# Performance work log

Hardware: AMD Instinct MI355X
Metric: run time of the kernel (lower is better)

## Reference

```python
import jax, jax.numpy as jnp
import numpy as np


def _coord1d(n):
    # make_coord: grid-center coordinates in (-1, 1)
    return -1.0 + 1.0 / n + (2.0 / n) * jnp.arange(n, dtype=jnp.float32)


def _conv1x1(x, w, b):
    # 1x1 conv == channel matmul. x: [B,C,H,W], w: [O,C], b: [O]
    return jnp.einsum('bchw,oc->bohw', x, w) + b[None, :, None, None]


def setup_inputs() -> dict:
    key = jax.random.key(0)
    ks = jax.random.split(key, 8)
    B, C, h, w = 2, 64, 96, 96
    d = 256
    Cin = (C + 2) * 4 + 2  # 266
    s = lambda k, shp, fan: (jax.random.normal(k, shp, jnp.float32) / np.sqrt(fan)).astype(jnp.float32)
    return {
        'feat': jax.random.normal(ks[0], (B, C, h, w), jnp.float32),
        'w00': s(ks[1], (d, Cin), Cin), 'b00': jnp.zeros((d,), jnp.float32),
        'w1': s(ks[2], (d, d), d), 'b1': jnp.zeros((d,), jnp.float32),
        'w2': s(ks[3], (3, d), d), 'b2': jnp.zeros((3,), jnp.float32),
        'ws1': s(ks[4], (C, C), C), 'bs1': jnp.zeros((C,), jnp.float32),
        'ws2': s(ks[5], (3, C), C), 'bs2': jnp.zeros((3,), jnp.float32),
        'target_h': 384, 'target_w': 384,
    }


def reference(feat, w00, b00, w1, b1, w2, b2, ws1, bs1, ws2, bs2, target_h, target_w):
    B, C, h, w = feat.shape
    H, W = int(target_h), int(target_w)
    # HR query coordinates, shared across batch. cy along height (dim0), cx along width (dim1)
    cy = jnp.broadcast_to(_coord1d(H)[:, None], (H, W))
    cx = jnp.broadcast_to(_coord1d(W)[None, :], (H, W))
    rx = 1.0 / h  # = 2/h/2, half-pixel radius along height
    ry = 1.0 / w
    eps_shift = 1e-6

    def nearest(c, n):
        # grid_sample nearest, align_corners=False: unnormalize then round (half-to-even, as nearbyint)
        u = ((c + 1.0) * n - 1.0) / 2.0
        return jnp.clip(jnp.round(u).astype(jnp.int32), 0, n - 1)

    rel_coords, feat_s, areas = [], [], []
    for vx in (-1.0, 1.0):
        for vy in (-1.0, 1.0):
            sy = jnp.clip(cy + vx * rx + eps_shift, -1.0 + 1e-6, 1.0 - 1e-6)
            sx = jnp.clip(cx + vy * ry + eps_shift, -1.0 + 1e-6, 1.0 - 1e-6)
            iy = nearest(sy, h)  # [H,W]
            ix = nearest(sx, w)
            feat_s.append(feat[:, :, iy, ix])  # [B,C,H,W] gather
            # nearest-sampled LR pixel-center coords (what grid_sample(pos_lr,...) returns)
            old_y = -1.0 + 1.0 / h + (2.0 / h) * iy.astype(jnp.float32)
            old_x = -1.0 + 1.0 / w + (2.0 / w) * ix.astype(jnp.float32)
            rel_y = (cy - old_y) * h
            rel_x = (cx - old_x) * w
            rel_coords.append(jnp.stack([rel_y, rel_x], 0))  # [2,H,W]
            areas.append(jnp.abs(rel_y * rel_x) + 1e-9)

    tot = areas[0] + areas[1] + areas[2] + areas[3]
    # LIIF area swap: 0<->3, 1<->2
    areas = [areas[3], areas[2], areas[1], areas[0]]
    feat_s = [f * (a / tot)[None, None] for f, a in zip(feat_s, areas)]

    scale_h, scale_w = H / h, W / w
    cell_h = (2.0 / H) * max(scale_h / 4.0, 1.0) * h
    cell_w = (2.0 / W) * max(scale_w / 4.0, 1.0) * w
    rel_cell = jnp.broadcast_to(
        jnp.array([cell_h, cell_w], jnp.float32)[None, :, None, None], (B, 2, H, W))
    rels = jnp.broadcast_to(jnp.concatenate(rel_coords, 0)[None], (B, 8, H, W))
    grid = jnp.concatenate([rels, *feat_s, rel_cell], axis=1)  # [B,266,H,W]

    x = _conv1x1(grid, w00, b00)
    ret = _conv1x1(jax.nn.gelu(_conv1x1(x, w1, b1), approximate=False), w2, b2)

    # shortcut branch: 1x1 MLP on LR feat, then bilinear border sample at coord
    sc = _conv1x1(jax.nn.relu(_conv1x1(feat, ws1, bs1)), ws2, bs2)  # [B,3,h,w]
    uy = ((cy + 1.0) * h - 1.0) / 2.0
    ux = ((cx + 1.0) * w - 1.0) / 2.0
    y0 = jnp.floor(uy)
    x0 = jnp.floor(ux)
    wy = uy - y0
    wx = ux - x0
    y0i = jnp.clip(y0.astype(jnp.int32), 0, h - 1)
    y1i = jnp.clip(y0.astype(jnp.int32) + 1, 0, h - 1)
    x0i = jnp.clip(x0.astype(jnp.int32), 0, w - 1)
    x1i = jnp.clip(x0.astype(jnp.int32) + 1, 0, w - 1)
    samp = (sc[:, :, y0i, x0i] * ((1 - wy) * (1 - wx))[None, None]
            + sc[:, :, y0i, x1i] * ((1 - wy) * wx)[None, None]
            + sc[:, :, y1i, x0i] * (wy * (1 - wx))[None, None]
            + sc[:, :, y1i, x1i] * (wy * wx)[None, None])
    return ret + samp
```

## Files before the change

kernel.cpp:

```cpp
#include <hip/hip_runtime.h>

typedef __bf16 bf16x8 __attribute__((ext_vector_type(8)));
typedef __bf16 bf16x4 __attribute__((ext_vector_type(4)));
typedef float f32x4 __attribute__((ext_vector_type(4)));

namespace {
constexpr int Bn = 2, Cn = 64, hn = 96, wn = 96, Hn = 384, Wn = 384;
constexpr int CIN = 266;
constexpr int TM = 64;
constexpr int SP = 296;
constexpr int L1_FRAGS = 9 * 16 * 64;
constexpr int L2_FRAGS = 8 * 16 * 64;
constexpr int L3_FRAGS = 8 * 64;
constexpr int N_FRAGS = L1_FRAGS + L2_FRAGS + L3_FRAGS;
constexpr int SC_OFF_BYTES = N_FRAGS * 16;
constexpr int B1EFF_OFF_BYTES = SC_OFF_BYTES + Bn * 3 * hn * wn * 4;
constexpr int FRAG_BLOCKS = N_FRAGS / 256;
constexpr int SC_BLOCKS = (Bn * hn * wn) / 256;
}

__global__ void prep_all(const float* __restrict__ w00, const float* __restrict__ w1,
                         const float* __restrict__ w2, const float* __restrict__ b00,
                         const float* __restrict__ b1,
                         const float* __restrict__ feat, const float* __restrict__ ws1,
                         const float* __restrict__ bs1, const float* __restrict__ ws2,
                         const float* __restrict__ bs2,
                         __bf16* __restrict__ wb, float* __restrict__ b1eff,
                         float* __restrict__ sc)
{
    const int bid = blockIdx.x;
    if (bid < FRAG_BLOCKS) {
        const int f = bid * 256 + threadIdx.x;
        bf16x8 v;
        if (f < L1_FRAGS) {
            const int k0 = f >> 10;
            const int mb = (f >> 6) & 15;
            const int l  = f & 63;
            const int m  = mb * 16 + (l & 15);
            const int kb = k0 * 32 + (l >> 4) * 8;
#pragma unroll
            for (int j = 0; j < 8; j++)
                v[j] = (kb + j < CIN) ? (__bf16)w00[m * CIN + kb + j] : (__bf16)0.f;
        } else if (f < L1_FRAGS + L2_FRAGS) {
            const int g = f - L1_FRAGS;
            const int k0 = g >> 10;
            const int mb = (g >> 6) & 15;
            const int l  = g & 63;
            const int m  = mb * 16 + (l & 15);
            const int kb = k0 * 32 + (l >> 4) * 8;
#pragma unroll
            for (int j = 0; j < 8; j++) v[j] = (__bf16)w1[m * 256 + kb + j];
        } else {
            const int g = f - (L1_FRAGS + L2_FRAGS);
            const int k0 = g >> 6;
            const int l  = g & 63;
            const int m  = l & 15;
            const int kb = k0 * 32 + (l >> 4) * 8;
#pragma unroll
            for (int j = 0; j < 8; j++)
                v[j] = (m < 3) ? (__bf16)w2[m * 256 + kb + j] : (__bf16)0.f;
        }
        *(bf16x8*)(wb + f * 8) = v;
        return;
    }
    if (bid == FRAG_BLOCKS) {
        __shared__ float cb[256];
        const int o = threadIdx.x;
        cb[o] = b00[o] + 0.5f * (w00[o * CIN + 264] + w00[o * CIN + 265]);
        __syncthreads();
        float v = b1[o];
#pragma unroll 4
        for (int k = 0; k < 256; k++) v = fmaf(w1[o * 256 + k], cb[k], v);
        b1eff[o] = v;
        return;
    }
    const int t = (bid - FRAG_BLOCKS - 1) * 256 + threadIdx.x;
    if (t >= Bn * hn * wn) return;
    const int b = t / (hn * wn);
    const int yx = t % (hn * wn);
    const float* fp = feat + b * Cn * hn * wn + yx;
    float f[Cn];
#pragma unroll
    for (int c = 0; c < Cn; c++) f[c] = fp[c * hn * wn];
    float o0 = bs2[0], o1 = bs2[1], o2 = bs2[2];
#pragma unroll 1
    for (int co = 0; co < Cn; co += 4) {
        float v0 = bs1[co], v1 = bs1[co + 1], v2 = bs1[co + 2], v3 = bs1[co + 3];
        const float* wr = ws1 + co * Cn;
#pragma unroll
        for (int ci = 0; ci < Cn; ci++) {
            const float fv = f[ci];
            v0 = fmaf(wr[ci], fv, v0);
            v1 = fmaf(wr[Cn + ci], fv, v1);
            v2 = fmaf(wr[2 * Cn + ci], fv, v2);
            v3 = fmaf(wr[3 * Cn + ci], fv, v3);
        }
        v0 = fmaxf(v0, 0.f); v1 = fmaxf(v1, 0.f); v2 = fmaxf(v2, 0.f); v3 = fmaxf(v3, 0.f);
#pragma unroll
        for (int u = 0; u < 4; u++) {
            const float vv = (u == 0) ? v0 : (u == 1) ? v1 : (u == 2) ? v2 : v3;
            o0 = fmaf(ws2[co + u], vv, o0);
            o1 = fmaf(ws2[Cn + co + u], vv, o1);
            o2 = fmaf(ws2[2 * Cn + co + u], vv, o2);
        }
    }
    sc[(b * 3 + 0) * hn * wn + yx] = o0;
    sc[(b * 3 + 1) * hn * wn + yx] = o1;
    sc[(b * 3 + 2) * hn * wn + yx] = o2;
}

__device__ __forceinline__ float gelu_fast(float x) {
    const float d0 = -2.302118074f;
    const float d1 = -0.1029453754f;
    float t = x * x;
    float a = x * fmaf(t, d1, d0);
    float e = __builtin_amdgcn_exp2f(a);
    return x * __builtin_amdgcn_rcpf(1.f + e);
}

__device__ __forceinline__ bf16x4 pack4(f32x4 x) {
    bf16x4 v;
    v[0] = (__bf16)x[0]; v[1] = (__bf16)x[1]; v[2] = (__bf16)x[2]; v[3] = (__bf16)x[3];
    return v;
}


#define MF(A, B, C) __builtin_amdgcn_mfma_f32_16x16x32_bf16((A), (B), (C), 0, 0, 0)

#define GSTEP(k0, W0, W1, W2, W3) do {                                          \
    const bf16x8 g0 = *(const bf16x8*)&Abuf[     lane16][(k0) * 32 + quad * 8]; \
    const bf16x8 g1 = *(const bf16x8*)&Abuf[16 + lane16][(k0) * 32 + quad * 8]; \
    const bf16x8 g2 = *(const bf16x8*)&Abuf[32 + lane16][(k0) * 32 + quad * 8]; \
    const bf16x8 g3 = *(const bf16x8*)&Abuf[48 + lane16][(k0) * 32 + quad * 8]; \
    a00 = MF(W0, g0, a00); a01 = MF(W1, g0, a01); a02 = MF(W2, g0, a02); a03 = MF(W3, g0, a03); \
    a10 = MF(W0, g1, a10); a11 = MF(W1, g1, a11); a12 = MF(W2, g1, a12); a13 = MF(W3, g1, a13); \
    a20 = MF(W0, g2, a20); a21 = MF(W1, g2, a21); a22 = MF(W2, g2, a22); a23 = MF(W3, g2, a23); \
    a30 = MF(W0, g3, a30); a31 = MF(W1, g3, a31); a32 = MF(W2, g3, a32); a33 = MF(W3, g3, a33); \
} while (0)

#define LDW(W0, W1, W2, W3, src, kk) do {             \
    W0 = (src)[((kk) * 16 + mb0 + 0) * 64 + lane];    \
    W1 = (src)[((kk) * 16 + mb0 + 1) * 64 + lane];    \
    W2 = (src)[((kk) * 16 + mb0 + 2) * 64 + lane];    \
    W3 = (src)[((kk) * 16 + mb0 + 3) * 64 + lane];    \
} while (0)

#define ZACC4(n) a##n##0 = zf; a##n##1 = zf; a##n##2 = zf; a##n##3 = zf

__global__ __launch_bounds__(256, 3) void liif_main(
    const float* __restrict__ feat, const float* __restrict__ b1eff,
    const float* __restrict__ b2v, const __bf16* __restrict__ wb,
    const float* __restrict__ sc, float* __restrict__ out)
{
    __shared__ __align__(16) __bf16 Abuf[TM][SP];

    const int t = threadIdx.x;
    const int wv = t >> 6;
    const int lane = t & 63;
    const int lane16 = lane & 15;
    const int quad = lane >> 4;
    const int mb0 = wv * 4;

    constexpr int NWG = Bn * Hn * (Wn / TM);
    const int lt = (blockIdx.x & 7) * (NWG / 8) + (blockIdx.x >> 3);
    constexpr int TPR = Wn / TM;
    const int tx = lt % TPR;
    const int Y = (lt / TPR) % Hn;
    const int b = lt / (TPR * Hn);
    const int X0 = tx * TM;

    const float cy = -1.f + 1.f / Hn + (2.f / Hn) * (float)Y;

    const bf16x8* wf1 = (const bf16x8*)wb;
    const bf16x8* wf2 = wf1 + L1_FRAGS;
    const bf16x8* w2f = wf1 + (L1_FRAGS + L2_FRAGS);

    bf16x8 wE0, wE1, wE2, wE3, wO0, wO1, wO2, wO3;
    LDW(wE0, wE1, wE2, wE3, wf1, 0);
    LDW(wO0, wO1, wO2, wO3, wf1, 1);

    {
        const int p = lane;
        const int j = wv;
        const int X = X0 + p;
        const float cx = -1.f + 1.f / Wn + (2.f / Wn) * (float)X;
        float rely[4], relx[4], area[4];
        int iyv[4], ixv[4];
#pragma unroll
        for (int c = 0; c < 4; c++) {
            const float vx = (c & 2) ? 1.f : -1.f;
            const float vy = (c & 1) ? 1.f : -1.f;
            float sy = fminf(fmaxf(cy + vx * (1.f / hn) + 1e-6f, -1.f + 1e-6f), 1.f - 1e-6f);
            float sx = fminf(fmaxf(cx + vy * (1.f / wn) + 1e-6f, -1.f + 1e-6f), 1.f - 1e-6f);
            float uy = ((sy + 1.f) * hn - 1.f) * 0.5f;
            float ux = ((sx + 1.f) * wn - 1.f) * 0.5f;
            int iy = min(max((int)rintf(uy), 0), hn - 1);
            int ix = min(max((int)rintf(ux), 0), wn - 1);
            float oy = -1.f + 1.f / hn + (2.f / hn) * (float)iy;
            float ox = -1.f + 1.f / wn + (2.f / wn) * (float)ix;
            rely[c] = (cy - oy) * hn;
            relx[c] = (cx - ox) * wn;
            area[c] = fabsf(rely[c] * relx[c]) + 1e-9f;
            iyv[c] = iy; ixv[c] = ix;
        }
        const float tot = area[0] + area[1] + area[2] + area[3];
        const float wj = area[3 - j] / tot;

        if (j == 0) {
            bf16x8 v;
#pragma unroll
            for (int c = 0; c < 4; c++) { v[2 * c] = (__bf16)rely[c]; v[2 * c + 1] = (__bf16)relx[c]; }
            *(bf16x8*)&Abuf[p][0] = v;
        }
        const float* fb = feat + ((b * Cn) * hn + iyv[j]) * wn + ixv[j];
#pragma unroll
        for (int c8 = 0; c8 < 8; c8++) {
            bf16x8 v;
#pragma unroll
            for (int cc = 0; cc < 8; cc++)
                v[cc] = (__bf16)(fb[(c8 * 8 + cc) * (hn * wn)] * wj);
            *(bf16x8*)&Abuf[p][8 + 64 * j + c8 * 8] = v;
        }
        if (j == 3) {
            bf16x8 z;
#pragma unroll
            for (int cc = 0; cc < 8; cc++) z[cc] = (__bf16)0.f;
            *(bf16x8*)&Abuf[p][264] = z;
            *(bf16x8*)&Abuf[p][272] = z;
            *(bf16x8*)&Abuf[p][280] = z;
        }
    }
    __syncthreads();

    const f32x4 zf = (f32x4){0.f, 0.f, 0.f, 0.f};
    f32x4 a00, a01, a02, a03, a10, a11, a12, a13;
    f32x4 a20, a21, a22, a23, a30, a31, a32, a33;
    ZACC4(0); ZACC4(1); ZACC4(2); ZACC4(3);

    GSTEP(0, wE0, wE1, wE2, wE3); LDW(wE0, wE1, wE2, wE3, wf1, 2);
    GSTEP(1, wO0, wO1, wO2, wO3); LDW(wO0, wO1, wO2, wO3, wf1, 3);
    GSTEP(2, wE0, wE1, wE2, wE3); LDW(wE0, wE1, wE2, wE3, wf1, 4);
    GSTEP(3, wO0, wO1, wO2, wO3); LDW(wO0, wO1, wO2, wO3, wf1, 5);
    GSTEP(4, wE0, wE1, wE2, wE3); LDW(wE0, wE1, wE2, wE3, wf1, 6);
    GSTEP(5, wO0, wO1, wO2, wO3); LDW(wO0, wO1, wO2, wO3, wf1, 7);
    GSTEP(6, wE0, wE1, wE2, wE3); LDW(wE0, wE1, wE2, wE3, wf1, 8);
    GSTEP(7, wO0, wO1, wO2, wO3); LDW(wO0, wO1, wO2, wO3, wf2, 0);
    GSTEP(8, wE0, wE1, wE2, wE3); LDW(wE0, wE1, wE2, wE3, wf2, 1);

    __syncthreads();
    {
        const int ch0 = mb0 * 16 + quad * 4;
        *(bf16x4*)&Abuf[     lane16][ch0     ] = pack4(a00);
        *(bf16x4*)&Abuf[16 + lane16][ch0     ] = pack4(a10);
        *(bf16x4*)&Abuf[32 + lane16][ch0     ] = pack4(a20);
        *(bf16x4*)&Abuf[48 + lane16][ch0     ] = pack4(a30);
        *(bf16x4*)&Abuf[     lane16][ch0 + 16] = pack4(a01);
        *(bf16x4*)&Abuf[16 + lane16][ch0 + 16] = pack4(a11);
        *(bf16x4*)&Abuf[32 + lane16][ch0 + 16] = pack4(a21);
        *(bf16x4*)&Abuf[48 + lane16][ch0 + 16] = pack4(a31);
        *(bf16x4*)&Abuf[     lane16][ch0 + 32] = pack4(a02);
        *(bf16x4*)&Abuf[16 + lane16][ch0 + 32] = pack4(a12);
        *(bf16x4*)&Abuf[32 + lane16][ch0 + 32] = pack4(a22);
        *(bf16x4*)&Abuf[48 + lane16][ch0 + 32] = pack4(a32);
        *(bf16x4*)&Abuf[     lane16][ch0 + 48] = pack4(a03);
        *(bf16x4*)&Abuf[16 + lane16][ch0 + 48] = pack4(a13);
        *(bf16x4*)&Abuf[32 + lane16][ch0 + 48] = pack4(a23);
        *(bf16x4*)&Abuf[48 + lane16][ch0 + 48] = pack4(a33);
    }
    __syncthreads();

    ZACC4(0); ZACC4(1); ZACC4(2); ZACC4(3);

    GSTEP(0, wO0, wO1, wO2, wO3); LDW(wO0, wO1, wO2, wO3, wf2, 2);
    GSTEP(1, wE0, wE1, wE2, wE3); LDW(wE0, wE1, wE2, wE3, wf2, 3);
    GSTEP(2, wO0, wO1, wO2, wO3); LDW(wO0, wO1, wO2, wO3, wf2, 4);
    GSTEP(3, wE0, wE1, wE2, wE3); LDW(wE0, wE1, wE2, wE3, wf2, 5);
    GSTEP(4, wO0, wO1, wO2, wO3); LDW(wO0, wO1, wO2, wO3, wf2, 6);
    GSTEP(5, wE0, wE1, wE2, wE3); LDW(wE0, wE1, wE2, wE3, wf2, 7);
    GSTEP(6, wO0, wO1, wO2, wO3); wO0 = w2f[0 * 64 + lane];
    GSTEP(7, wE0, wE1, wE2, wE3); wE0 = w2f[1 * 64 + lane];

    __syncthreads();
    {
        const int ch0 = mb0 * 16 + quad * 4;
        const f32x4 bi0 = *(const f32x4*)&b1eff[ch0];
        const f32x4 bi1 = *(const f32x4*)&b1eff[ch0 + 16];
        const f32x4 bi2 = *(const f32x4*)&b1eff[ch0 + 32];
        const f32x4 bi3 = *(const f32x4*)&b1eff[ch0 + 48];
#define GEL4(x, bi) { bf16x4 v; v[0] = (__bf16)gelu_fast((x)[0] + (bi)[0]); \
        v[1] = (__bf16)gelu_fast((x)[1] + (bi)[1]); \
        v[2] = (__bf16)gelu_fast((x)[2] + (bi)[2]); \
        v[3] = (__bf16)gelu_fast((x)[3] + (bi)[3]); vv = v; }
        bf16x4 vv;
        GEL4(a00, bi0); *(bf16x4*)&Abuf[     lane16][ch0     ] = vv;
        GEL4(a10, bi0); *(bf16x4*)&Abuf[16 + lane16][ch0     ] = vv;
        GEL4(a20, bi0); *(bf16x4*)&Abuf[32 + lane16][ch0     ] = vv;
        GEL4(a30, bi0); *(bf16x4*)&Abuf[48 + lane16][ch0     ] = vv;
        GEL4(a01, bi1); *(bf16x4*)&Abuf[     lane16][ch0 + 16] = vv;
        GEL4(a11, bi1); *(bf16x4*)&Abuf[16 + lane16][ch0 + 16] = vv;
        GEL4(a21, bi1); *(bf16x4*)&Abuf[32 + lane16][ch0 + 16] = vv;
        GEL4(a31, bi1); *(bf16x4*)&Abuf[48 + lane16][ch0 + 16] = vv;
        GEL4(a02, bi2); *(bf16x4*)&Abuf[     lane16][ch0 + 32] = vv;
        GEL4(a12, bi2); *(bf16x4*)&Abuf[16 + lane16][ch0 + 32] = vv;
        GEL4(a22, bi2); *(bf16x4*)&Abuf[32 + lane16][ch0 + 32] = vv;
        GEL4(a32, bi2); *(bf16x4*)&Abuf[48 + lane16][ch0 + 32] = vv;
        GEL4(a03, bi3); *(bf16x4*)&Abuf[     lane16][ch0 + 48] = vv;
        GEL4(a13, bi3); *(bf16x4*)&Abuf[16 + lane16][ch0 + 48] = vv;
        GEL4(a23, bi3); *(bf16x4*)&Abuf[32 + lane16][ch0 + 48] = vv;
        GEL4(a33, bi3); *(bf16x4*)&Abuf[48 + lane16][ch0 + 48] = vv;
#undef GEL4
    }
    __syncthreads();

    f32x4 acc3 = zf;
#define YF(k0) (*(const bf16x8*)&Abuf[wv * 16 + lane16][(k0) * 32 + quad * 8])
    acc3 = MF(wO0, YF(0), acc3); wO0 = w2f[2 * 64 + lane];
    acc3 = MF(wE0, YF(1), acc3); wE0 = w2f[3 * 64 + lane];
    acc3 = MF(wO0, YF(2), acc3); wO0 = w2f[4 * 64 + lane];
    acc3 = MF(wE0, YF(3), acc3); wE0 = w2f[5 * 64 + lane];
    acc3 = MF(wO0, YF(4), acc3); wO0 = w2f[6 * 64 + lane];
    acc3 = MF(wE0, YF(5), acc3); wE0 = w2f[7 * 64 + lane];
    acc3 = MF(wO0, YF(6), acc3);
    acc3 = MF(wE0, YF(7), acc3);
#undef YF

    if (quad == 0) {
        const int pix = wv * 16 + lane16;
        const int X = X0 + pix;
        const float uy = ((cy + 1.f) * hn - 1.f) * 0.5f;
        const float fy = floorf(uy);
        const float wy = uy - fy;
        const int y0i = min(max((int)fy, 0), hn - 1);
        const int y1i = min(max((int)fy + 1, 0), hn - 1);
        const float cx = -1.f + 1.f / Wn + (2.f / Wn) * (float)X;
        const float ux = ((cx + 1.f) * wn - 1.f) * 0.5f;
        const float fx = floorf(ux);
        const float wx = ux - fx;
        const int x0i = min(max((int)fx, 0), wn - 1);
        const int x1i = min(max((int)fx + 1, 0), wn - 1);
        const float w00b = (1.f - wy) * (1.f - wx), w01b = (1.f - wy) * wx;
        const float w10b = wy * (1.f - wx), w11b = wy * wx;
#pragma unroll
        for (int r = 0; r < 3; r++) {
            const float* scb = sc + (b * 3 + r) * (hn * wn);
            const float samp = scb[y0i * wn + x0i] * w00b + scb[y0i * wn + x1i] * w01b
                             + scb[y1i * wn + x0i] * w10b + scb[y1i * wn + x1i] * w11b;
            out[((b * 3 + r) * Hn + Y) * Wn + X] = acc3[r] + b2v[r] + samp;
        }
    }
}

extern "C" void kernel_launch(void* const* d_in, const int* in_sizes, int n_in,
                              void* d_out, int out_size, void* d_ws, size_t ws_size,
                              hipStream_t stream)
{
    const float* feat = (const float*)d_in[0];
    const float* w00  = (const float*)d_in[1];
    const float* b00  = (const float*)d_in[2];
    const float* w1   = (const float*)d_in[3];
    const float* b1   = (const float*)d_in[4];
    const float* w2   = (const float*)d_in[5];
    const float* b2   = (const float*)d_in[6];
    const float* ws1  = (const float*)d_in[7];
    const float* bs1  = (const float*)d_in[8];
    const float* ws2  = (const float*)d_in[9];
    const float* bs2  = (const float*)d_in[10];
    float* out = (float*)d_out;

    __bf16* wb    = (__bf16*)d_ws;
    float* scbuf  = (float*)((char*)d_ws + SC_OFF_BYTES);
    float* b1eff  = (float*)((char*)d_ws + B1EFF_OFF_BYTES);

    prep_all<<<FRAG_BLOCKS + 1 + SC_BLOCKS, 256, 0, stream>>>(
        w00, w1, w2, b00, b1, feat, ws1, bs1, ws2, bs2, wb, b1eff, scbuf);
    liif_main<<<Bn * Hn * (Wn / TM), 256, 0, stream>>>(feat, b1eff, b2, wb, scbuf, out);
}
```

Before: 198.5 us.

## Split main kernel across eight waves with half the accumulators each

Raises the main kernel's block from 256 to 512 threads (8 waves). Each wave now owns 2 of the 16-column output blocks instead of 4, which halves accumulator and weight-fragment registers per wave, and the gather is split so each wave loads half the channels. Launch bounds move to (512,4) so more waves can be resident to hide latency. The trade-offs are that each wave reloads the shared LDS activations for half the MFMA work, and only 4 of the 8 waves do the final 3-output layer and epilogue.

```diff
diff --git a/kernel.cpp b/kernel.cpp
--- a/kernel.cpp
+++ b/kernel.cpp
@@ -16,7 +16,8 @@
 constexpr int SC_OFF_BYTES = N_FRAGS * 16;
 constexpr int B1EFF_OFF_BYTES = SC_OFF_BYTES + Bn * 3 * hn * wn * 4;
 constexpr int FRAG_BLOCKS = N_FRAGS / 256;
-constexpr int SC_BLOCKS = (Bn * hn * wn) / 256;
+constexpr int NPIX = Bn * hn * wn;
+constexpr int SC_BLOCKS = NPIX / 256;
 }
 
 __global__ void prep_all(const float* __restrict__ w00, const float* __restrict__ w1,
@@ -75,7 +76,7 @@
         return;
     }
     const int t = (bid - FRAG_BLOCKS - 1) * 256 + threadIdx.x;
-    if (t >= Bn * hn * wn) return;
+    if (t >= NPIX) return;
     const int b = t / (hn * wn);
     const int yx = t % (hn * wn);
     const float* fp = feat + b * Cn * hn * wn + yx;
@@ -127,27 +128,23 @@
 
 #define MF(A, B, C) __builtin_amdgcn_mfma_f32_16x16x32_bf16((A), (B), (C), 0, 0, 0)
 
-#define GSTEP(k0, W0, W1, W2, W3) do {                                          \
+#define GSTEP(k0, W0, W1) do {                                                  \
     const bf16x8 g0 = *(const bf16x8*)&Abuf[     lane16][(k0) * 32 + quad * 8]; \
     const bf16x8 g1 = *(const bf16x8*)&Abuf[16 + lane16][(k0) * 32 + quad * 8]; \
     const bf16x8 g2 = *(const bf16x8*)&Abuf[32 + lane16][(k0) * 32 + quad * 8]; \
     const bf16x8 g3 = *(const bf16x8*)&Abuf[48 + lane16][(k0) * 32 + quad * 8]; \
-    a00 = MF(W0, g0, a00); a01 = MF(W1, g0, a01); a02 = MF(W2, g0, a02); a03 = MF(W3, g0, a03); \
-    a10 = MF(W0, g1, a10); a11 = MF(W1, g1, a11); a12 = MF(W2, g1, a12); a13 = MF(W3, g1, a13); \
-    a20 = MF(W0, g2, a20); a21 = MF(W1, g2, a21); a22 = MF(W2, g2, a22); a23 = MF(W3, g2, a23); \
-    a30 = MF(W0, g3, a30); a31 = MF(W1, g3, a31); a32 = MF(W2, g3, a32); a33 = MF(W3, g3, a33); \
+    a00 = MF(W0, g0, a00); a01 = MF(W1, g0, a01);                               \
+    a10 = MF(W0, g1, a10); a11 = MF(W1, g1, a11);                               \
+    a20 = MF(W0, g2, a20); a21 = MF(W1, g2, a21);                               \
+    a30 = MF(W0, g3, a30); a31 = MF(W1, g3, a31);                               \
 } while (0)
 
-#define LDW(W0, W1, W2, W3, src, kk) do {             \
-    W0 = (src)[((kk) * 16 + mb0 + 0) * 64 + lane];    \
-    W1 = (src)[((kk) * 16 + mb0 + 1) * 64 + lane];    \
-    W2 = (src)[((kk) * 16 + mb0 + 2) * 64 + lane];    \
-    W3 = (src)[((kk) * 16 + mb0 + 3) * 64 + lane];    \
+#define LDW(W0, W1, src, kk) do {                       \
+    W0 = (src)[((kk) * 16 + mb0 + 0) * 64 + lane];      \
+    W1 = (src)[((kk) * 16 + mb0 + 1) * 64 + lane];      \
 } while (0)
 
-#define ZACC4(n) a##n##0 = zf; a##n##1 = zf; a##n##2 = zf; a##n##3 = zf
-
-__global__ __launch_bounds__(256, 3) void liif_main(
+__global__ __launch_bounds__(512, 4) void liif_main(
     const float* __restrict__ feat, const float* __restrict__ b1eff,
     const float* __restrict__ b2v, const __bf16* __restrict__ wb,
     const float* __restrict__ sc, float* __restrict__ out)
@@ -159,7 +156,7 @@
     const int lane = t & 63;
     const int lane16 = lane & 15;
     const int quad = lane >> 4;
-    const int mb0 = wv * 4;
+    const int mb0 = wv * 2;
 
     constexpr int NWG = Bn * Hn * (Wn / TM);
     const int lt = (blockIdx.x & 7) * (NWG / 8) + (blockIdx.x >> 3);
@@ -175,13 +172,10 @@
     const bf16x8* wf2 = wf1 + L1_FRAGS;
     const bf16x8* w2f = wf1 + (L1_FRAGS + L2_FRAGS);
 
-    bf16x8 wE0, wE1, wE2, wE3, wO0, wO1, wO2, wO3;
-    LDW(wE0, wE1, wE2, wE3, wf1, 0);
-    LDW(wO0, wO1, wO2, wO3, wf1, 1);
-
     {
         const int p = lane;
-        const int j = wv;
+        const int j = wv & 3;
+        const int half = wv >> 2;
         const int X = X0 + p;
         const float cx = -1.f + 1.f / Wn + (2.f / Wn) * (float)X;
         float rely[4], relx[4], area[4];
@@ -206,22 +200,22 @@
         const float tot = area[0] + area[1] + area[2] + area[3];
         const float wj = area[3 - j] / tot;
 
-        if (j == 0) {
+        if (wv == 0) {
             bf16x8 v;
 #pragma unroll
             for (int c = 0; c < 4; c++) { v[2 * c] = (__bf16)rely[c]; v[2 * c + 1] = (__bf16)relx[c]; }
             *(bf16x8*)&Abuf[p][0] = v;
         }
-        const float* fb = feat + ((b * Cn) * hn + iyv[j]) * wn + ixv[j];
-#pragma unroll
-        for (int c8 = 0; c8 < 8; c8++) {
+        const float* fb = feat + ((b * Cn + half * 32) * hn + iyv[j]) * wn + ixv[j];
+#pragma unroll
+        for (int c8 = 0; c8 < 4; c8++) {
             bf16x8 v;
 #pragma unroll
             for (int cc = 0; cc < 8; cc++)
                 v[cc] = (__bf16)(fb[(c8 * 8 + cc) * (hn * wn)] * wj);
-            *(bf16x8*)&Abuf[p][8 + 64 * j + c8 * 8] = v;
-        }
-        if (j == 3) {
+            *(bf16x8*)&Abuf[p][8 + 64 * j + half * 32 + c8 * 8] = v;
+        }
+        if (wv == 3) {
             bf16x8 z;
 #pragma unroll
             for (int cc = 0; cc < 8; cc++) z[cc] = (__bf16)0.f;
@@ -230,22 +224,25 @@
             *(bf16x8*)&Abuf[p][280] = z;
         }
     }
+
+    bf16x8 wE0, wE1, wO0, wO1;
+    LDW(wE0, wE1, wf1, 0);
+    LDW(wO0, wO1, wf1, 1);
     __syncthreads();
 
     const f32x4 zf = (f32x4){0.f, 0.f, 0.f, 0.f};
-    f32x4 a00, a01, a02, a03, a10, a11, a12, a13;
-    f32x4 a20, a21, a22, a23, a30, a31, a32, a33;
-    ZACC4(0); ZACC4(1); ZACC4(2); ZACC4(3);
-
-    GSTEP(0, wE0, wE1, wE2, wE3); LDW(wE0, wE1, wE2, wE3, wf1, 2);
-    GSTEP(1, wO0, wO1, wO2, wO3); LDW(wO0, wO1, wO2, wO3, wf1, 3);
-    GSTEP(2, wE0, wE1, wE2, wE3); LDW(wE0, wE1, wE2, wE3, wf1, 4);
-    GSTEP(3, wO0, wO1, wO2, wO3); LDW(wO0, wO1, wO2, wO3, wf1, 5);
-    GSTEP(4, wE0, wE1, wE2, wE3); LDW(wE0, wE1, wE2, wE3, wf1, 6);
-    GSTEP(5, wO0, wO1, wO2, wO3); LDW(wO0, wO1, wO2, wO3, wf1, 7);
-    GSTEP(6, wE0, wE1, wE2, wE3); LDW(wE0, wE1, wE2, wE3, wf1, 8);
-    GSTEP(7, wO0, wO1, wO2, wO3); LDW(wO0, wO1, wO2, wO3, wf2, 0);
-    GSTEP(8, wE0, wE1, wE2, wE3); LDW(wE0, wE1, wE2, wE3, wf2, 1);
+    f32x4 a00, a01, a10, a11, a20, a21, a30, a31;
+    a00 = zf; a01 = zf; a10 = zf; a11 = zf; a20 = zf; a21 = zf; a30 = zf; a31 = zf;
+
+    GSTEP(0, wE0, wE1); LDW(wE0, wE1, wf1, 2);
+    GSTEP(1, wO0, wO1); LDW(wO0, wO1, wf1, 3);
+    GSTEP(2, wE0, wE1); LDW(wE0, wE1, wf1, 4);
+    GSTEP(3, wO0, wO1); LDW(wO0, wO1, wf1, 5);
+    GSTEP(4, wE0, wE1); LDW(wE0, wE1, wf1, 6);
+    GSTEP(5, wO0, wO1); LDW(wO0, wO1, wf1, 7);
+    GSTEP(6, wE0, wE1); LDW(wE0, wE1, wf1, 8);
+    GSTEP(7, wO0, wO1); LDW(wO0, wO1, wf2, 0);
+    GSTEP(8, wE0, wE1); LDW(wE0, wE1, wf2, 1);
 
     __syncthreads();
     {
@@ -258,35 +255,25 @@
         *(bf16x4*)&Abuf[16 + lane16][ch0 + 16] = pack4(a11);
         *(bf16x4*)&Abuf[32 + lane16][ch0 + 16] = pack4(a21);
         *(bf16x4*)&Abuf[48 + lane16][ch0 + 16] = pack4(a31);
-        *(bf16x4*)&Abuf[     lane16][ch0 + 32] = pack4(a02);
-        *(bf16x4*)&Abuf[16 + lane16][ch0 + 32] = pack4(a12);
-        *(bf16x4*)&Abuf[32 + lane16][ch0 + 32] = pack4(a22);
-        *(bf16x4*)&Abuf[48 + lane16][ch0 + 32] = pack4(a32);
-        *(bf16x4*)&Abuf[     lane16][ch0 + 48] = pack4(a03);
-        *(bf16x4*)&Abuf[16 + lane16][ch0 + 48] = pack4(a13);
-        *(bf16x4*)&Abuf[32 + lane16][ch0 + 48] = pack4(a23);
-        *(bf16x4*)&Abuf[48 + lane16][ch0 + 48] = pack4(a33);
-    }
-    __syncthreads();
-
-    ZACC4(0); ZACC4(1); ZACC4(2); ZACC4(3);
-
-    GSTEP(0, wO0, wO1, wO2, wO3); LDW(wO0, wO1, wO2, wO3, wf2, 2);
-    GSTEP(1, wE0, wE1, wE2, wE3); LDW(wE0, wE1, wE2, wE3, wf2, 3);
-    GSTEP(2, wO0, wO1, wO2, wO3); LDW(wO0, wO1, wO2, wO3, wf2, 4);
-    GSTEP(3, wE0, wE1, wE2, wE3); LDW(wE0, wE1, wE2, wE3, wf2, 5);
-    GSTEP(4, wO0, wO1, wO2, wO3); LDW(wO0, wO1, wO2, wO3, wf2, 6);
-    GSTEP(5, wE0, wE1, wE2, wE3); LDW(wE0, wE1, wE2, wE3, wf2, 7);
-    GSTEP(6, wO0, wO1, wO2, wO3); wO0 = w2f[0 * 64 + lane];
-    GSTEP(7, wE0, wE1, wE2, wE3); wE0 = w2f[1 * 64 + lane];
+    }
+    __syncthreads();
+
+    a00 = zf; a01 = zf; a10 = zf; a11 = zf; a20 = zf; a21 = zf; a30 = zf; a31 = zf;
+
+    GSTEP(0, wO0, wO1); LDW(wO0, wO1, wf2, 2);
+    GSTEP(1, wE0, wE1); LDW(wE0, wE1, wf2, 3);
+    GSTEP(2, wO0, wO1); LDW(wO0, wO1, wf2, 4);
+    GSTEP(3, wE0, wE1); LDW(wE0, wE1, wf2, 5);
+    GSTEP(4, wO0, wO1); LDW(wO0, wO1, wf2, 6);
+    GSTEP(5, wE0, wE1); LDW(wE0, wE1, wf2, 7);
+    GSTEP(6, wO0, wO1); wO0 = w2f[0 * 64 + lane];
+    GSTEP(7, wE0, wE1); wE0 = w2f[1 * 64 + lane];
 
     __syncthreads();
     {
         const int ch0 = mb0 * 16 + quad * 4;
         const f32x4 bi0 = *(const f32x4*)&b1eff[ch0];
         const f32x4 bi1 = *(const f32x4*)&b1eff[ch0 + 16];
-        const f32x4 bi2 = *(const f32x4*)&b1eff[ch0 + 32];
-        const f32x4 bi3 = *(const f32x4*)&b1eff[ch0 + 48];
 #define GEL4(x, bi) { bf16x4 v; v[0] = (__bf16)gelu_fast((x)[0] + (bi)[0]); \
         v[1] = (__bf16)gelu_fast((x)[1] + (bi)[1]); \
         v[2] = (__bf16)gelu_fast((x)[2] + (bi)[2]); \
@@ -300,52 +287,46 @@
         GEL4(a11, bi1); *(bf16x4*)&Abuf[16 + lane16][ch0 + 16] = vv;
         GEL4(a21, bi1); *(bf16x4*)&Abuf[32 + lane16][ch0 + 16] = vv;
         GEL4(a31, bi1); *(bf16x4*)&Abuf[48 + lane16][ch0 + 16] = vv;
-        GEL4(a02, bi2); *(bf16x4*)&Abuf[     lane16][ch0 + 32] = vv;
-        GEL4(a12, bi2); *(bf16x4*)&Abuf[16 + lane16][ch0 + 32] = vv;
-        GEL4(a22, bi2); *(bf16x4*)&Abuf[32 + lane16][ch0 + 32] = vv;
-        GEL4(a32, bi2); *(bf16x4*)&Abuf[48 + lane16][ch0 + 32] = vv;
-        GEL4(a03, bi3); *(bf16x4*)&Abuf[     lane16][ch0 + 48] = vv;
-        GEL4(a13, bi3); *(bf16x4*)&Abuf[16 + lane16][ch0 + 48] = vv;
-        GEL4(a23, bi3); *(bf16x4*)&Abuf[32 + lane16][ch0 + 48] = vv;
-        GEL4(a33, bi3); *(bf16x4*)&Abuf[48 + lane16][ch0 + 48] = vv;
 #undef GEL4
     }
     __syncthreads();
 
-    f32x4 acc3 = zf;
+    if (wv < 4) {
+        f32x4 acc3 = zf;
 #define YF(k0) (*(const bf16x8*)&Abuf[wv * 16 + lane16][(k0) * 32 + quad * 8])
-    acc3 = MF(wO0, YF(0), acc3); wO0 = w2f[2 * 64 + lane];
-    acc3 = MF(wE0, YF(1), acc3); wE0 = w2f[3 * 64 + lane];
-    acc3 = MF(wO0, YF(2), acc3); wO0 = w2f[4 * 64 + lane];
-    acc3 = MF(wE0, YF(3), acc3); wE0 = w2f[5 * 64 + lane];
-    acc3 = MF(wO0, YF(4), acc3); wO0 = w2f[6 * 64 + lane];
-    acc3 = MF(wE0, YF(5), acc3); wE0 = w2f[7 * 64 + lane];
-    acc3 = MF(wO0, YF(6), acc3);
-    acc3 = MF(wE0, YF(7), acc3);
+        acc3 = MF(wO0, YF(0), acc3); wO0 = w2f[2 * 64 + lane];
+        acc3 = MF(wE0, YF(1), acc3); wE0 = w2f[3 * 64 + lane];
+        acc3 = MF(wO0, YF(2), acc3); wO0 = w2f[4 * 64 + lane];
+        acc3 = MF(wE0, YF(3), acc3); wE0 = w2f[5 * 64 + lane];
+        acc3 = MF(wO0, YF(4), acc3); wO0 = w2f[6 * 64 + lane];
+        acc3 = MF(wE0, YF(5), acc3); wE0 = w2f[7 * 64 + lane];
+        acc3 = MF(wO0, YF(6), acc3);
+        acc3 = MF(wE0, YF(7), acc3);
 #undef YF
 
-    if (quad == 0) {
-        const int pix = wv * 16 + lane16;
-        const int X = X0 + pix;
-        const float uy = ((cy + 1.f) * hn - 1.f) * 0.5f;
-        const float fy = floorf(uy);
-        const float wy = uy - fy;
-        const int y0i = min(max((int)fy, 0), hn - 1);
-        const int y1i = min(max((int)fy + 1, 0), hn - 1);
-        const float cx = -1.f + 1.f / Wn + (2.f / Wn) * (float)X;
-        const float ux = ((cx + 1.f) * wn - 1.f) * 0.5f;
-        const float fx = floorf(ux);
-        const float wx = ux - fx;
-        const int x0i = min(max((int)fx, 0), wn - 1);
-        const int x1i = min(max((int)fx + 1, 0), wn - 1);
-        const float w00b = (1.f - wy) * (1.f - wx), w01b = (1.f - wy) * wx;
-        const float w10b = wy * (1.f - wx), w11b = wy * wx;
-#pragma unroll
-        for (int r = 0; r < 3; r++) {
-            const float* scb = sc + (b * 3 + r) * (hn * wn);
-            const float samp = scb[y0i * wn + x0i] * w00b + scb[y0i * wn + x1i] * w01b
-                             + scb[y1i * wn + x0i] * w10b + scb[y1i * wn + x1i] * w11b;
-            out[((b * 3 + r) * Hn + Y) * Wn + X] = acc3[r] + b2v[r] + samp;
+        if (quad == 0) {
+            const int pix = wv * 16 + lane16;
+            const int X = X0 + pix;
+            const float uy = ((cy + 1.f) * hn - 1.f) * 0.5f;
+            const float fy = floorf(uy);
+            const float wy = uy - fy;
+            const int y0i = min(max((int)fy, 0), hn - 1);
+            const int y1i = min(max((int)fy + 1, 0), hn - 1);
+            const float cx = -1.f + 1.f / Wn + (2.f / Wn) * (float)X;
+            const float ux = ((cx + 1.f) * wn - 1.f) * 0.5f;
+            const float fx = floorf(ux);
+            const float wx = ux - fx;
+            const int x0i = min(max((int)fx, 0), wn - 1);
+            const int x1i = min(max((int)fx + 1, 0), wn - 1);
+            const float w00b = (1.f - wy) * (1.f - wx), w01b = (1.f - wy) * wx;
+            const float w10b = wy * (1.f - wx), w11b = wy * wx;
+#pragma unroll
+            for (int r = 0; r < 3; r++) {
+                const float* scb = sc + (b * 3 + r) * (hn * wn);
+                const float samp = scb[y0i * wn + x0i] * w00b + scb[y0i * wn + x1i] * w01b
+                                 + scb[y1i * wn + x0i] * w10b + scb[y1i * wn + x1i] * w11b;
+                out[((b * 3 + r) * Hn + Y) * Wn + X] = acc3[r] + b2v[r] + samp;
+            }
         }
     }
 }
@@ -373,5 +354,5 @@
 
     prep_all<<<FRAG_BLOCKS + 1 + SC_BLOCKS, 256, 0, stream>>>(
         w00, w1, w2, b00, b1, feat, ws1, bs1, ws2, bs2, wb, b1eff, scbuf);
-    liif_main<<<Bn * Hn * (Wn / TM), 256, 0, stream>>>(feat, b1eff, b2, wb, scbuf, out);
-}
+    liif_main<<<Bn * Hn * (Wn / TM), 512, 0, stream>>>(feat, b1eff, b2, wb, scbuf, out);
+}
```

Result: slower. 209.6 us (+5.6%).

## Split LDS activation rows into two halves and software-pipeline A-fragment loads

Applied to the files above, without the earlier changes.

Reorganises the shared-memory activation tile so each 8-element k-fragment is stored as two 4-element halves placed 144 columns apart. The intent is to change the LDS bank-access pattern of the MFMA operand reads. The GEMM steps also prefetch the next k-step's first two A fragments while issuing the current MFMAs, overlapping LDS latency with matrix work. Every producer (gather, GELU writeback, intermediate writeback) and consumer (all three GEMMs) has to follow the new index mapping, which adds addressing complexity and some register pressure.

```diff
diff --git a/kernel.cpp b/kernel.cpp
--- a/kernel.cpp
+++ b/kernel.cpp
@@ -16,8 +16,10 @@
 constexpr int SC_OFF_BYTES = N_FRAGS * 16;
 constexpr int B1EFF_OFF_BYTES = SC_OFF_BYTES + Bn * 3 * hn * wn * 4;
 constexpr int FRAG_BLOCKS = N_FRAGS / 256;
-constexpr int SC_BLOCKS = (Bn * hn * wn) / 256;
-}
+constexpr int NPIX = Bn * hn * wn;
+constexpr int SC_BLOCKS = NPIX / 256;
+}
+
 
 __global__ void prep_all(const float* __restrict__ w00, const float* __restrict__ w1,
                          const float* __restrict__ w2, const float* __restrict__ b00,
@@ -75,7 +77,7 @@
         return;
     }
     const int t = (bid - FRAG_BLOCKS - 1) * 256 + threadIdx.x;
-    if (t >= Bn * hn * wn) return;
+    if (t >= NPIX) return;
     const int b = t / (hn * wn);
     const int yx = t % (hn * wn);
     const float* fp = feat + b * Cn * hn * wn + yx;
@@ -124,18 +126,28 @@
     return v;
 }
 
-
 #define MF(A, B, C) __builtin_amdgcn_mfma_f32_16x16x32_bf16((A), (B), (C), 0, 0, 0)
 
-#define GSTEP(k0, W0, W1, W2, W3) do {                                          \
-    const bf16x8 g0 = *(const bf16x8*)&Abuf[     lane16][(k0) * 32 + quad * 8]; \
-    const bf16x8 g1 = *(const bf16x8*)&Abuf[16 + lane16][(k0) * 32 + quad * 8]; \
-    const bf16x8 g2 = *(const bf16x8*)&Abuf[32 + lane16][(k0) * 32 + quad * 8]; \
-    const bf16x8 g3 = *(const bf16x8*)&Abuf[48 + lane16][(k0) * 32 + quad * 8]; \
-    a00 = MF(W0, g0, a00); a01 = MF(W1, g0, a01); a02 = MF(W2, g0, a02); a03 = MF(W3, g0, a03); \
-    a10 = MF(W0, g1, a10); a11 = MF(W1, g1, a11); a12 = MF(W2, g1, a12); a13 = MF(W3, g1, a13); \
-    a20 = MF(W0, g2, a20); a21 = MF(W1, g2, a21); a22 = MF(W2, g2, a22); a23 = MF(W3, g2, a23); \
-    a30 = MF(W0, g3, a30); a31 = MF(W1, g3, a31); a32 = MF(W2, g3, a32); a33 = MF(W3, g3, a33); \
+#define LD1(D, R, k0) do {                                                      \
+    *(bf16x4*)&D         = *(const bf16x4*)&Abuf[R][(k0) * 16 + q4];            \
+    *(((bf16x4*)&D) + 1) = *(const bf16x4*)&Abuf[R][144 + (k0) * 16 + q4];      \
+} while (0)
+
+#define LDG2(P0, P1, k0) do { LD1(P0, lane16, k0); LD1(P1, 16 + lane16, k0); } while (0)
+
+#define GSTP(W0, W1, W2, W3, G0, G1, k0, N0, N1, knx, NXP) do {                 \
+    bf16x8 Gt2, Gt3;                                                            \
+    LD1(Gt2, 32 + lane16, k0);                                                  \
+    LD1(Gt3, 48 + lane16, k0);                                                  \
+    if (NXP) { LDG2(N0, N1, knx); }                                             \
+    a00 = MF(W0, G0, a00); a01 = MF(W1, G0, a01);                               \
+    a02 = MF(W2, G0, a02); a03 = MF(W3, G0, a03);                               \
+    a10 = MF(W0, G1, a10); a11 = MF(W1, G1, a11);                               \
+    a12 = MF(W2, G1, a12); a13 = MF(W3, G1, a13);                               \
+    a20 = MF(W0, Gt2, a20); a21 = MF(W1, Gt2, a21);                             \
+    a22 = MF(W2, Gt2, a22); a23 = MF(W3, Gt2, a23);                             \
+    a30 = MF(W0, Gt3, a30); a31 = MF(W1, Gt3, a31);                             \
+    a32 = MF(W2, Gt3, a32); a33 = MF(W3, Gt3, a33);                             \
 } while (0)
 
 #define LDW(W0, W1, W2, W3, src, kk) do {             \
@@ -159,6 +171,7 @@
     const int lane = t & 63;
     const int lane16 = lane & 15;
     const int quad = lane >> 4;
+    const int q4 = quad * 4;
     const int mb0 = wv * 4;
 
     constexpr int NWG = Bn * Hn * (Wn / TM);
@@ -207,27 +220,35 @@
         const float wj = area[3 - j] / tot;
 
         if (j == 0) {
-            bf16x8 v;
-#pragma unroll
-            for (int c = 0; c < 4; c++) { v[2 * c] = (__bf16)rely[c]; v[2 * c + 1] = (__bf16)relx[c]; }
-            *(bf16x8*)&Abuf[p][0] = v;
+            bf16x4 lo, hi;
+            lo[0] = (__bf16)rely[0]; lo[1] = (__bf16)relx[0];
+            lo[2] = (__bf16)rely[1]; lo[3] = (__bf16)relx[1];
+            hi[0] = (__bf16)rely[2]; hi[1] = (__bf16)relx[2];
+            hi[2] = (__bf16)rely[3]; hi[3] = (__bf16)relx[3];
+            *(bf16x4*)&Abuf[p][0]   = lo;
+            *(bf16x4*)&Abuf[p][144] = hi;
         }
         const float* fb = feat + ((b * Cn) * hn + iyv[j]) * wn + ixv[j];
 #pragma unroll
         for (int c8 = 0; c8 < 8; c8++) {
-            bf16x8 v;
-#pragma unroll
-            for (int cc = 0; cc < 8; cc++)
-                v[cc] = (__bf16)(fb[(c8 * 8 + cc) * (hn * wn)] * wj);
-            *(bf16x8*)&Abuf[p][8 + 64 * j + c8 * 8] = v;
+            bf16x4 lo, hi;
+#pragma unroll
+            for (int cc = 0; cc < 4; cc++)
+                lo[cc] = (__bf16)(fb[(c8 * 8 + cc) * (hn * wn)] * wj);
+#pragma unroll
+            for (int cc = 4; cc < 8; cc++)
+                hi[cc - 4] = (__bf16)(fb[(c8 * 8 + cc) * (hn * wn)] * wj);
+            const int tq = 1 + 8 * j + c8;
+            const int cb = (tq >> 2) * 16 + (tq & 3) * 4;
+            *(bf16x4*)&Abuf[p][cb]       = lo;
+            *(bf16x4*)&Abuf[p][144 + cb] = hi;
         }
         if (j == 3) {
-            bf16x8 z;
-#pragma unroll
-            for (int cc = 0; cc < 8; cc++) z[cc] = (__bf16)0.f;
-            *(bf16x8*)&Abuf[p][264] = z;
-            *(bf16x8*)&Abuf[p][272] = z;
-            *(bf16x8*)&Abuf[p][280] = z;
+            bf16x4 z;
+            z[0] = (__bf16)0.f; z[1] = (__bf16)0.f; z[2] = (__bf16)0.f; z[3] = (__bf16)0.f;
+            *(bf16x4*)&Abuf[p][132] = z; *(bf16x4*)&Abuf[p][276] = z;
+            *(bf16x4*)&Abuf[p][136] = z; *(bf16x4*)&Abuf[p][280] = z;
+            *(bf16x4*)&Abuf[p][140] = z; *(bf16x4*)&Abuf[p][284] = z;
         }
     }
     __syncthreads();
@@ -237,92 +258,105 @@
     f32x4 a20, a21, a22, a23, a30, a31, a32, a33;
     ZACC4(0); ZACC4(1); ZACC4(2); ZACC4(3);
 
-    GSTEP(0, wE0, wE1, wE2, wE3); LDW(wE0, wE1, wE2, wE3, wf1, 2);
-    GSTEP(1, wO0, wO1, wO2, wO3); LDW(wO0, wO1, wO2, wO3, wf1, 3);
-    GSTEP(2, wE0, wE1, wE2, wE3); LDW(wE0, wE1, wE2, wE3, wf1, 4);
-    GSTEP(3, wO0, wO1, wO2, wO3); LDW(wO0, wO1, wO2, wO3, wf1, 5);
-    GSTEP(4, wE0, wE1, wE2, wE3); LDW(wE0, wE1, wE2, wE3, wf1, 6);
-    GSTEP(5, wO0, wO1, wO2, wO3); LDW(wO0, wO1, wO2, wO3, wf1, 7);
-    GSTEP(6, wE0, wE1, wE2, wE3); LDW(wE0, wE1, wE2, wE3, wf1, 8);
-    GSTEP(7, wO0, wO1, wO2, wO3); LDW(wO0, wO1, wO2, wO3, wf2, 0);
-    GSTEP(8, wE0, wE1, wE2, wE3); LDW(wE0, wE1, wE2, wE3, wf2, 1);
+    bf16x8 gE0, gE1, gO0, gO1;
+    LDG2(gE0, gE1, 0);
+
+    GSTP(wE0, wE1, wE2, wE3, gE0, gE1, 0, gO0, gO1, 1, 1); LDW(wE0, wE1, wE2, wE3, wf1, 2);
+    GSTP(wO0, wO1, wO2, wO3, gO0, gO1, 1, gE0, gE1, 2, 1); LDW(wO0, wO1, wO2, wO3, wf1, 3);
+    GSTP(wE0, wE1, wE2, wE3, gE0, gE1, 2, gO0, gO1, 3, 1); LDW(wE0, wE1, wE2, wE3, wf1, 4);
+    GSTP(wO0, wO1, wO2, wO3, gO0, gO1, 3, gE0, gE1, 4, 1); LDW(wO0, wO1, wO2, wO3, wf1, 5);
+    GSTP(wE0, wE1, wE2, wE3, gE0, gE1, 4, gO0, gO1, 5, 1); LDW(wE0, wE1, wE2, wE3, wf1, 6);
+    GSTP(wO0, wO1, wO2, wO3, gO0, gO1, 5, gE0, gE1, 6, 1); LDW(wO0, wO1, wO2, wO3, wf1, 7);
+    GSTP(wE0, wE1, wE2, wE3, gE0, gE1, 6, gO0, gO1, 7, 1); LDW(wE0, wE1, wE2, wE3, wf1, 8);
+    GSTP(wO0, wO1, wO2, wO3, gO0, gO1, 7, gE0, gE1, 8, 1); LDW(wO0, wO1, wO2, wO3, wf2, 0);
+    GSTP(wE0, wE1, wE2, wE3, gE0, gE1, 8, gO0, gO1, 0, 0); LDW(wE0, wE1, wE2, wE3, wf2, 1);
 
     __syncthreads();
     {
-        const int ch0 = mb0 * 16 + quad * 4;
-        *(bf16x4*)&Abuf[     lane16][ch0     ] = pack4(a00);
-        *(bf16x4*)&Abuf[16 + lane16][ch0     ] = pack4(a10);
-        *(bf16x4*)&Abuf[32 + lane16][ch0     ] = pack4(a20);
-        *(bf16x4*)&Abuf[48 + lane16][ch0     ] = pack4(a30);
-        *(bf16x4*)&Abuf[     lane16][ch0 + 16] = pack4(a01);
-        *(bf16x4*)&Abuf[16 + lane16][ch0 + 16] = pack4(a11);
-        *(bf16x4*)&Abuf[32 + lane16][ch0 + 16] = pack4(a21);
-        *(bf16x4*)&Abuf[48 + lane16][ch0 + 16] = pack4(a31);
-        *(bf16x4*)&Abuf[     lane16][ch0 + 32] = pack4(a02);
-        *(bf16x4*)&Abuf[16 + lane16][ch0 + 32] = pack4(a12);
-        *(bf16x4*)&Abuf[32 + lane16][ch0 + 32] = pack4(a22);
-        *(bf16x4*)&Abuf[48 + lane16][ch0 + 32] = pack4(a32);
-        *(bf16x4*)&Abuf[     lane16][ch0 + 48] = pack4(a03);
-        *(bf16x4*)&Abuf[16 + lane16][ch0 + 48] = pack4(a13);
-        *(bf16x4*)&Abuf[32 + lane16][ch0 + 48] = pack4(a23);
-        *(bf16x4*)&Abuf[48 + lane16][ch0 + 48] = pack4(a33);
+        const int qb = quad & 1, qh = quad >> 1;
+        const int ce = 144 * qb + qh * 4;
+        const int co = 144 * qb + (2 + qh) * 4;
+        const int r16 = wv * 32;
+        *(bf16x4*)&Abuf[     lane16][ce + r16]      = pack4(a00);
+        *(bf16x4*)&Abuf[16 + lane16][ce + r16]      = pack4(a10);
+        *(bf16x4*)&Abuf[32 + lane16][ce + r16]      = pack4(a20);
+        *(bf16x4*)&Abuf[48 + lane16][ce + r16]      = pack4(a30);
+        *(bf16x4*)&Abuf[     lane16][co + r16]      = pack4(a01);
+        *(bf16x4*)&Abuf[16 + lane16][co + r16]      = pack4(a11);
+        *(bf16x4*)&Abuf[32 + lane16][co + r16]      = pack4(a21);
+        *(bf16x4*)&Abuf[48 + lane16][co + r16]      = pack4(a31);
+        *(bf16x4*)&Abuf[     lane16][ce + r16 + 16] = pack4(a02);
+        *(bf16x4*)&Abuf[16 + lane16][ce + r16 + 16] = pack4(a12);
+        *(bf16x4*)&Abuf[32 + lane16][ce + r16 + 16] = pack4(a22);
+        *(bf16x4*)&Abuf[48 + lane16][ce + r16 + 16] = pack4(a32);
+        *(bf16x4*)&Abuf[     lane16][co + r16 + 16] = pack4(a03);
+        *(bf16x4*)&Abuf[16 + lane16][co + r16 + 16] = pack4(a13);
+        *(bf16x4*)&Abuf[32 + lane16][co + r16 + 16] = pack4(a23);
+        *(bf16x4*)&Abuf[48 + lane16][co + r16 + 16] = pack4(a33);
     }
     __syncthreads();
 
     ZACC4(0); ZACC4(1); ZACC4(2); ZACC4(3);
-
-    GSTEP(0, wO0, wO1, wO2, wO3); LDW(wO0, wO1, wO2, wO3, wf2, 2);
-    GSTEP(1, wE0, wE1, wE2, wE3); LDW(wE0, wE1, wE2, wE3, wf2, 3);
-    GSTEP(2, wO0, wO1, wO2, wO3); LDW(wO0, wO1, wO2, wO3, wf2, 4);
-    GSTEP(3, wE0, wE1, wE2, wE3); LDW(wE0, wE1, wE2, wE3, wf2, 5);
-    GSTEP(4, wO0, wO1, wO2, wO3); LDW(wO0, wO1, wO2, wO3, wf2, 6);
-    GSTEP(5, wE0, wE1, wE2, wE3); LDW(wE0, wE1, wE2, wE3, wf2, 7);
-    GSTEP(6, wO0, wO1, wO2, wO3); wO0 = w2f[0 * 64 + lane];
-    GSTEP(7, wE0, wE1, wE2, wE3); wE0 = w2f[1 * 64 + lane];
+    LDG2(gE0, gE1, 0);
+
+    GSTP(wO0, wO1, wO2, wO3, gE0, gE1, 0, gO0, gO1, 1, 1); LDW(wO0, wO1, wO2, wO3, wf2, 2);
+    GSTP(wE0, wE1, wE2, wE3, gO0, gO1, 1, gE0, gE1, 2, 1); LDW(wE0, wE1, wE2, wE3, wf2, 3);
+    GSTP(wO0, wO1, wO2, wO3, gE0, gE1, 2, gO0, gO1, 3, 1); LDW(wO0, wO1, wO2, wO3, wf2, 4);
+    GSTP(wE0, wE1, wE2, wE3, gO0, gO1, 3, gE0, gE1, 4, 1); LDW(wE0, wE1, wE2, wE3, wf2, 5);
+    GSTP(wO0, wO1, wO2, wO3, gE0, gE1, 4, gO0, gO1, 5, 1); LDW(wO0, wO1, wO2, wO3, wf2, 6);
+    GSTP(wE0, wE1, wE2, wE3, gO0, gO1, 5, gE0, gE1, 6, 1); LDW(wE0, wE1, wE2, wE3, wf2, 7);
+    GSTP(wO0, wO1, wO2, wO3, gE0, gE1, 6, gO0, gO1, 7, 1); wO0 = w2f[0 * 64 + lane];
+    GSTP(wE0, wE1, wE2, wE3, gO0, gO1, 7, gE0, gE1, 0, 0); wE0 = w2f[1 * 64 + lane];
 
     __syncthreads();
     {
-        const int ch0 = mb0 * 16 + quad * 4;
-        const f32x4 bi0 = *(const f32x4*)&b1eff[ch0];
-        const f32x4 bi1 = *(const f32x4*)&b1eff[ch0 + 16];
-        const f32x4 bi2 = *(const f32x4*)&b1eff[ch0 + 32];
-        const f32x4 bi3 = *(const f32x4*)&b1eff[ch0 + 48];
+        const int qb = quad & 1, qh = quad >> 1;
+        const int ce = 144 * qb + qh * 4;
+        const int co = 144 * qb + (2 + qh) * 4;
+        const int r16 = wv * 32;
 #define GEL4(x, bi) { bf16x4 v; v[0] = (__bf16)gelu_fast((x)[0] + (bi)[0]); \
         v[1] = (__bf16)gelu_fast((x)[1] + (bi)[1]); \
         v[2] = (__bf16)gelu_fast((x)[2] + (bi)[2]); \
         v[3] = (__bf16)gelu_fast((x)[3] + (bi)[3]); vv = v; }
         bf16x4 vv;
-        GEL4(a00, bi0); *(bf16x4*)&Abuf[     lane16][ch0     ] = vv;
-        GEL4(a10, bi0); *(bf16x4*)&Abuf[16 + lane16][ch0     ] = vv;
-        GEL4(a20, bi0); *(bf16x4*)&Abuf[32 + lane16][ch0     ] = vv;
-        GEL4(a30, bi0); *(bf16x4*)&Abuf[48 + lane16][ch0     ] = vv;
-        GEL4(a01, bi1); *(bf16x4*)&Abuf[     lane16][ch0 + 16] = vv;
-        GEL4(a11, bi1); *(bf16x4*)&Abuf[16 + lane16][ch0 + 16] = vv;
-        GEL4(a21, bi1); *(bf16x4*)&Abuf[32 + lane16][ch0 + 16] = vv;
-        GEL4(a31, bi1); *(bf16x4*)&Abuf[48 + lane16][ch0 + 16] = vv;
-        GEL4(a02, bi2); *(bf16x4*)&Abuf[     lane16][ch0 + 32] = vv;
-        GEL4(a12, bi2); *(bf16x4*)&Abuf[16 + lane16][ch0 + 32] = vv;
-        GEL4(a22, bi2); *(bf16x4*)&Abuf[32 + lane16][ch0 + 32] = vv;
-        GEL4(a32, bi2); *(bf16x4*)&Abuf[48 + lane16][ch0 + 32] = vv;
-        GEL4(a03, bi3); *(bf16x4*)&Abuf[     lane16][ch0 + 48] = vv;
-        GEL4(a13, bi3); *(bf16x4*)&Abuf[16 + lane16][ch0 + 48] = vv;
-        GEL4(a23, bi3); *(bf16x4*)&Abuf[32 + lane16][ch0 + 48] = vv;
-        GEL4(a33, bi3); *(bf16x4*)&Abuf[48 + lane16][ch0 + 48] = vv;
+        const f32x4 bi0 = *(const f32x4*)&b1eff[(mb0 + 0) * 16 + q4];
+        const f32x4 bi1 = *(const f32x4*)&b1eff[(mb0 + 1) * 16 + q4];
+        const f32x4 bi2 = *(const f32x4*)&b1eff[(mb0 + 2) * 16 + q4];
+        const f32x4 bi3 = *(const f32x4*)&b1eff[(mb0 + 3) * 16 + q4];
+        GEL4(a00, bi0); *(bf16x4*)&Abuf[     lane16][ce + r16]      = vv;
+        GEL4(a10, bi0); *(bf16x4*)&Abuf[16 + lane16][ce + r16]      = vv;
+        GEL4(a20, bi0); *(bf16x4*)&Abuf[32 + lane16][ce + r16]      = vv;
+        GEL4(a30, bi0); *(bf16x4*)&Abuf[48 + lane16][ce + r16]      = vv;
+        GEL4(a01, bi1); *(bf16x4*)&Abuf[     lane16][co + r16]      = vv;
+        GEL4(a11, bi1); *(bf16x4*)&Abuf[16 + lane16][co + r16]      = vv;
+        GEL4(a21, bi1); *(bf16x4*)&Abuf[32 + lane16][co + r16]      = vv;
+        GEL4(a31, bi1); *(bf16x4*)&Abuf[48 + lane16][co + r16]      = vv;
+        GEL4(a02, bi2); *(bf16x4*)&Abuf[     lane16][ce + r16 + 16] = vv;
+        GEL4(a12, bi2); *(bf16x4*)&Abuf[16 + lane16][ce + r16 + 16] = vv;
+        GEL4(a22, bi2); *(bf16x4*)&Abuf[32 + lane16][ce + r16 + 16] = vv;
+        GEL4(a32, bi2); *(bf16x4*)&Abuf[48 + lane16][ce + r16 + 16] = vv;
+        GEL4(a03, bi3); *(bf16x4*)&Abuf[     lane16][co + r16 + 16] = vv;
+        GEL4(a13, bi3); *(bf16x4*)&Abuf[16 + lane16][co + r16 + 16] = vv;
+        GEL4(a23, bi3); *(bf16x4*)&Abuf[32 + lane16][co + r16 + 16] = vv;
+        GEL4(a33, bi3); *(bf16x4*)&Abuf[48 + lane16][co + r16 + 16] = vv;
 #undef GEL4
     }
     __syncthreads();
 
     f32x4 acc3 = zf;
-#define YF(k0) (*(const bf16x8*)&Abuf[wv * 16 + lane16][(k0) * 32 + quad * 8])
-    acc3 = MF(wO0, YF(0), acc3); wO0 = w2f[2 * 64 + lane];
-    acc3 = MF(wE0, YF(1), acc3); wE0 = w2f[3 * 64 + lane];
-    acc3 = MF(wO0, YF(2), acc3); wO0 = w2f[4 * 64 + lane];
-    acc3 = MF(wE0, YF(3), acc3); wE0 = w2f[5 * 64 + lane];
-    acc3 = MF(wO0, YF(4), acc3); wO0 = w2f[6 * 64 + lane];
-    acc3 = MF(wE0, YF(5), acc3); wE0 = w2f[7 * 64 + lane];
-    acc3 = MF(wO0, YF(6), acc3);
-    acc3 = MF(wE0, YF(7), acc3);
-#undef YF
+    {
+        const int row3 = wv * 16 + lane16;
+        bf16x8 y0, y1;
+        LD1(y0, row3, 0);
+        LD1(y1, row3, 1); acc3 = MF(wO0, y0, acc3); wO0 = w2f[2 * 64 + lane];
+        LD1(y0, row3, 2); acc3 = MF(wE0, y1, acc3); wE0 = w2f[3 * 64 + lane];
+        LD1(y1, row3, 3); acc3 = MF(wO0, y0, acc3); wO0 = w2f[4 * 64 + lane];
+        LD1(y0, row3, 4); acc3 = MF(wE0, y1, acc3); wE0 = w2f[5 * 64 + lane];
+        LD1(y1, row3, 5); acc3 = MF(wO0, y0, acc3); wO0 = w2f[6 * 64 + lane];
+        LD1(y0, row3, 6); acc3 = MF(wE0, y1, acc3); wE0 = w2f[7 * 64 + lane];
+        LD1(y1, row3, 7); acc3 = MF(wO0, y0, acc3);
+                          acc3 = MF(wE0, y1, acc3);
+    }
 
     if (quad == 0) {
         const int pix = wv * 16 + lane16;
```

Result: slower. 218.1 us (+9.8%).
